# Optimization experiments

Measured on AMD Instinct MI355X. Metric: run time of the kernel, lower is better.

## Reference

```python
import jax, jax.numpy as jnp
import numpy as np

B, C, H, W = 4, 128, 256, 256
N, NPOS, KS = 4000, 8, 3
CH = 2 * NPOS  # mask=False -> 2*n_pos offset channels


def setup_inputs() -> dict:
    key = jax.random.key(0)
    ks = jax.random.split(key, 8)
    x = jax.random.normal(ks[0], (B, C, H, W), jnp.float32)
    keypoints = jax.random.uniform(ks[1], (B, N, 2), jnp.float32) * 2.0 - 1.0  # [-1,1]
    w1 = jax.random.normal(ks[2], (CH, C, KS, KS), jnp.float32) * 0.05  # offset conv 3x3
    b1 = jnp.zeros((CH,), jnp.float32)
    w2 = jax.random.normal(ks[3], (CH, CH), jnp.float32) * 0.05        # offset conv 1x1
    b2 = jnp.zeros((CH,), jnp.float32)
    wsf = jax.random.normal(ks[4], (C, C), jnp.float32) * 0.05         # sf_conv 1x1 no bias
    agg_weights = jax.random.uniform(ks[5], (NPOS, C, C), jnp.float32)  # torch.rand init
    return {"x": x, "keypoints": keypoints, "w1": w1, "b1": b1, "w2": w2,
            "b2": b2, "wsf": wsf, "agg_weights": agg_weights}


def _bilinear_sample(img, px, py):
    """grid_sample(mode=bilinear, align_corners=True, padding=zeros) at pixel coords.
    img: (C,H,W); px,py: (M,). Returns (C,M)."""
    c, h, w = img.shape
    x0f = jnp.floor(px); y0f = jnp.floor(py)
    x0 = x0f.astype(jnp.int32); y0 = y0f.astype(jnp.int32)
    wx1 = px - x0f; wx0 = 1.0 - wx1
    wy1 = py - y0f; wy0 = 1.0 - wy1

    def tap(xi, yi, wgt):
        valid = ((xi >= 0) & (xi < w) & (yi >= 0) & (yi < h)).astype(img.dtype)
        v = img[:, jnp.clip(yi, 0, h - 1), jnp.clip(xi, 0, w - 1)]  # (C,M)
        return v * (wgt * valid)

    return (tap(x0, y0, wx0 * wy0) + tap(x0 + 1, y0, wx1 * wy0)
            + tap(x0, y0 + 1, wx0 * wy1) + tap(x0 + 1, y0 + 1, wx1 * wy1))


def _per_image(xi, kpts, w1, b1, w2, b2, wsf, agg_weights):
    wh = jnp.array([W - 1.0, H - 1.0], xi.dtype)
    max_offset = max(H, W) / 4.0
    kwh = (kpts / 2.0 + 0.5) * wh                      # (N,2) pixel coords, >=0
    rc = kwh.astype(jnp.int32)                          # .long() trunc (positive)
    corner = jnp.trunc(rc.astype(jnp.float32) - KS / 2.0 + 1.0).astype(jnp.int32)
    cx = jnp.clip(corner[:, 0], 0, W - 1 - KS)
    cy = jnp.clip(corner[:, 1], 0, H - 1 - KS)
    ar = jnp.arange(KS)
    # patch[n,c,a,b] = xi[c, cy_n+a, cx_n+b]
    patch = xi[:, (cy[:, None] + ar)[:, :, None], (cx[:, None] + ar)[:, None, :]]  # (C,N,KS,KS)
    patch = patch.transpose(1, 0, 2, 3)                 # (N,C,KS,KS)
    # offset network: 3x3 conv (valid) on 3x3 patch == full contraction, then ReLU, 1x1 conv
    h1 = jax.nn.relu(jnp.einsum('nchw,ochw->no', patch, w1) + b1)
    off = jnp.clip(h1 @ w2.T + b2, -max_offset, max_offset)  # (N, 2*NPOS)
    off = off.reshape(-1, 2, NPOS).transpose(0, 2, 1)        # (N,NPOS,2)
    # deform sampling positions; torch normalizes then grid_sample(align_corners=True)
    # maps exactly back to pixel coords, so sample at pixel coords directly
    pos = kwh[:, None, :] + off                              # (N,NPOS,2)
    feats = _bilinear_sample(xi, pos[..., 0].reshape(-1), pos[..., 1].reshape(-1))  # (C,N*NPOS)
    feats = feats.reshape(C, -1, NPOS).transpose(1, 0, 2)    # (N,C,NPOS)
    feats = jax.nn.selu(jnp.einsum('ncp,dc->ndp', feats, wsf))
    descs = jnp.einsum('ncp,pcd->nd', feats, agg_weights)    # (N,C)
    descs = descs / jnp.maximum(jnp.linalg.norm(descs, axis=1, keepdims=True), 1e-12)
    return descs, off


def reference(x, keypoints, w1, b1, w2, b2, wsf, agg_weights):
    f = jax.vmap(lambda xi, k: _per_image(xi, k, w1, b1, w2, b2, wsf, agg_weights))
    descriptors, offsets = f(x, keypoints)
    return descriptors, offsets  # (B,N,C), (B,N,NPOS,2)
```

## Files before the change

kernel.cpp:

```cpp
#include <hip/hip_runtime.h>
#include <math.h>

#define BB 4
#define CC 128
#define HH 256
#define WW 256
#define NN 4000
#define NPOS 8
#define KS 3
#define HWSZ (HH*WW)

#define SELU_ALPHA 1.6732632423543772f
#define SELU_SCALE 1.0507009873554805f
#define MAX_OFFSET 64.0f

typedef unsigned short ushort_t;
typedef short short8 __attribute__((ext_vector_type(8)));
typedef float f32x4 __attribute__((ext_vector_type(4)));
typedef unsigned short ushort4_t __attribute__((ext_vector_type(4)));

#define XT_ELEMS    ((size_t)BB*HH*WW*CC)
#define WSFBF_ELEMS ((size_t)CC*CC)
#define AGGT_ELEMS  ((size_t)NPOS*CC*CC)
#define W1T_ELEMS   ((size_t)16*CC*9)
#define WS_NEEDED   ((XT_ELEMS+WSFBF_ELEMS+AGGT_ELEMS+W1T_ELEMS)*sizeof(ushort_t))

__device__ __forceinline__ ushort_t f2bf(float f) {
    unsigned u = __builtin_bit_cast(unsigned, f);
    unsigned r = (u + 0x7FFFu + ((u >> 16) & 1u)) >> 16;
    return (ushort_t)r;
}
__device__ __forceinline__ float bf2f(ushort_t u) {
    return __builtin_bit_cast(float, ((unsigned)u) << 16);
}

__global__ __launch_bounds__(256) void k0p(
    const float* __restrict__ x, ushort_t* __restrict__ xt,
    const float* __restrict__ wsf, const float* __restrict__ agg,
    const float* __restrict__ w1,
    ushort_t* __restrict__ wsf_bf, ushort_t* __restrict__ aggT_bf,
    ushort_t* __restrict__ w1t_bf)
{
    int blk = blockIdx.x;
    const int t = threadIdx.x;
    if (blk >= BB * HH * 4) {
        int i = (blk - BB * HH * 4) * 256 + t;
        if (i < CC * CC) wsf_bf[i] = f2bf(wsf[i]);
        if (i < NPOS * CC * CC) {
            int p = i >> 14, d = (i >> 7) & 127, c = i & 127;
            aggT_bf[i] = f2bf(agg[(p << 14) + (c << 7) + d]);
        }
        if (i < 16 * 1152) {
            int o = i / 1152, e = i - o * 1152, k = e >> 7, c = e & 127;
            w1t_bf[i] = f2bf(w1[o * 1152 + c * 9 + k]);
        }
        return;
    }
    int xc = blk & 3, y = (blk >> 2) & 255, b = blk >> 10;
    int x0 = xc * 64;
    __shared__ ushort_t lds[64][136];

    const float* xb = x + (size_t)b * CC * HWSZ + (size_t)y * WW + x0;
    for (int v = t; v < 2048; v += 256) {
        int c = v >> 4, xo4 = v & 15;
        float4 val = *(const float4*)(xb + (size_t)c * HWSZ + xo4 * 4);
        lds[xo4*4+0][c] = f2bf(val.x);
        lds[xo4*4+1][c] = f2bf(val.y);
        lds[xo4*4+2][c] = f2bf(val.z);
        lds[xo4*4+3][c] = f2bf(val.w);
    }
    __syncthreads();
    ushort_t* outb = xt + ((size_t)b * HWSZ + (size_t)y * WW + x0) * CC;
    for (int v = t; v < 2048; v += 256) {
        int xo = v >> 5, c4 = v & 31;
        ushort4_t val;
        val[0] = lds[xo][c4*4+0];
        val[1] = lds[xo][c4*4+1];
        val[2] = lds[xo][c4*4+2];
        val[3] = lds[xo][c4*4+3];
        *(ushort4_t*)(outb + (size_t)xo * CC + c4 * 4) = val;
    }
}

__global__ __launch_bounds__(256, 2) void k14_fused(
    const ushort_t* __restrict__ xt, const float* __restrict__ kpts,
    const ushort_t* __restrict__ w1t_bf, const float* __restrict__ b1,
    const float* __restrict__ w2, const float* __restrict__ b2,
    const ushort_t* __restrict__ wsf_bf, const ushort_t* __restrict__ aggT_bf,
    float* __restrict__ out_desc, float* __restrict__ out_off)
{
    const int t    = threadIdx.x;
    const int wv   = t >> 6;
    const int lane = t & 63;
    const int m    = lane & 15;
    const int q    = lane >> 4;
    const int n0   = blockIdx.x * 16;
    const int b    = n0 / NN;
    const ushort_t* xb = xt + (size_t)b * HWSZ * CC;

    __shared__ ushort_t feats[CC * CC];
    __shared__ ushort_t g[CC * CC];
    __shared__ union {
        struct {
            float partials[4][16][16];
            float h1f[16][17];
            float offs[16][16];
            int   tapoff[128][4];
            float tapw[128][4];
        } a;
        float dbuf[16 * 132];
    } u;
    __shared__ float kw[16][2];
    __shared__ int   cxy[16][2];
    __shared__ float rn[16];

    if (t < 16) {
        float kx = kpts[(size_t)(n0 + t) * 2 + 0];
        float ky = kpts[(size_t)(n0 + t) * 2 + 1];
        float kwx = (kx * 0.5f + 0.5f) * (float)(WW - 1);
        float kwy = (ky * 0.5f + 0.5f) * (float)(HH - 1);
        kw[t][0] = kwx; kw[t][1] = kwy;
        int rcx = (int)kwx, rcy = (int)kwy;
        int cx = (int)truncf((float)rcx - 0.5f);
        int cy = (int)truncf((float)rcy - 0.5f);
        cxy[t][0] = min(max(cx, 0), WW - 1 - KS);
        cxy[t][1] = min(max(cy, 0), HH - 1 - KS);
    }
    __syncthreads();

    {
        int px0 = cxy[m][0], py0 = cxy[m][1];
        f32x4 hacc = {0.f, 0.f, 0.f, 0.f};
        const ushort_t* brow = w1t_bf + m * 1152 + wv * 288 + q * 8;
        #pragma unroll
        for (int kk = 0; kk < 9; ++kk) {
            int e = wv * 288 + kk * 32 + q * 8;
            int k = e >> 7, c = e & 127;
            int kd = k / 3, kx2 = k - kd * 3;
            const ushort_t* src = xb + ((size_t)((py0 + kd) * WW + px0 + kx2)) * CC + c;
            short8 a   = *(const short8*)src;
            short8 bfr = *(const short8*)(brow + kk * 32);
            hacc = __builtin_amdgcn_mfma_f32_16x16x32_bf16(a, bfr, hacc, 0, 0, 0);
        }
        #pragma unroll
        for (int r = 0; r < 4; ++r) u.a.partials[wv][q * 4 + r][m] = hacc[r];
    }
    __syncthreads();
    {
        int kp = t >> 4, o = t & 15;
        float h = u.a.partials[0][kp][o] + u.a.partials[1][kp][o]
                + u.a.partials[2][kp][o] + u.a.partials[3][kp][o] + b1[o];
        u.a.h1f[kp][o] = fmaxf(h, 0.f);
    }
    __syncthreads();
    {
        int kp = t >> 4, j = t & 15;
        float s = b2[j];
        #pragma unroll
        for (int o = 0; o < 16; ++o) s += u.a.h1f[kp][o] * w2[j * 16 + o];
        s = fminf(fmaxf(s, -MAX_OFFSET), MAX_OFFSET);
        u.a.offs[kp][j] = s;
        int p = j & 7, comp = j >> 3;
        out_off[((size_t)(n0 + kp) * 8 + p) * 2 + comp] = s;
    }
    __syncthreads();

    if (t < 128) {
        int kp = t >> 3, p = t & 7;
        float px = kw[kp][0] + u.a.offs[kp][p];
        float py = kw[kp][1] + u.a.offs[kp][8 + p];
        float x0f = floorf(px), y0f = floorf(py);
        int x0 = (int)x0f, y0 = (int)y0f;
        float wx1 = px - x0f, wx0 = 1.f - wx1;
        float wy1 = py - y0f, wy0 = 1.f - wy1;
        int x0c = min(max(x0, 0), WW - 1);
        int x1c = min(max(x0 + 1, 0), WW - 1);
        int y0c = min(max(y0, 0), HH - 1);
        int y1c = min(max(y0 + 1, 0), HH - 1);
        float vx0 = (x0 >= 0 && x0 < WW) ? 1.f : 0.f;
        float vx1 = (x0 + 1 >= 0 && x0 + 1 < WW) ? 1.f : 0.f;
        float vy0 = (y0 >= 0 && y0 < HH) ? 1.f : 0.f;
        float vy1 = (y0 + 1 >= 0 && y0 + 1 < HH) ? 1.f : 0.f;
        u.a.tapoff[t][0] = (y0c * WW + x0c) * CC;
        u.a.tapoff[t][1] = (y0c * WW + x1c) * CC;
        u.a.tapoff[t][2] = (y1c * WW + x0c) * CC;
        u.a.tapoff[t][3] = (y1c * WW + x1c) * CC;
        u.a.tapw[t][0] = wx0 * wy0 * vx0 * vy0;
        u.a.tapw[t][1] = wx1 * wy0 * vx1 * vy0;
        u.a.tapw[t][2] = wx0 * wy1 * vx0 * vy1;
        u.a.tapw[t][3] = wx1 * wy1 * vx1 * vy1;
    }
    __syncthreads();

    {
        int pair = t >> 1, half = t & 1;
        const ushort_t* s0 = xb + u.a.tapoff[pair][0];
        const ushort_t* s1 = xb + u.a.tapoff[pair][1];
        const ushort_t* s2 = xb + u.a.tapoff[pair][2];
        const ushort_t* s3 = xb + u.a.tapoff[pair][3];
        float w00 = u.a.tapw[pair][0], w01 = u.a.tapw[pair][1];
        float w10 = u.a.tapw[pair][2], w11 = u.a.tapw[pair][3];
        unsigned rbase = (unsigned)(pair * 256);
        unsigned key   = ((unsigned)(pair & 7)) << 4;
        #pragma unroll
        for (int i = 0; i < 16; ++i) {
            int c = half * 64 + i * 4;
            ushort4_t t0 = *(const ushort4_t*)(s0 + c);
            ushort4_t t1 = *(const ushort4_t*)(s1 + c);
            ushort4_t t2 = *(const ushort4_t*)(s2 + c);
            ushort4_t t3 = *(const ushort4_t*)(s3 + c);
            ushort4_t r4;
            #pragma unroll
            for (int j = 0; j < 4; ++j) {
                float v = bf2f(t0[j]) * w00 + bf2f(t1[j]) * w01
                        + bf2f(t2[j]) * w10 + bf2f(t3[j]) * w11;
                r4[j] = f2bf(v);
            }
            unsigned byte = (rbase + (unsigned)c * 2) ^ key;
            *(ushort4_t*)((char*)feats + byte) = r4;
        }
    }
    __syncthreads();

    for (int rti = 0; rti < 2; ++rti) {
        int rt = wv * 2 + rti;
        int r  = rt * 16 + m;
        unsigned key = ((unsigned)(r & 7)) << 4;
        short8 afr[4];
        #pragma unroll
        for (int kk = 0; kk < 4; ++kk) {
            unsigned byte = ((unsigned)(r * 256 + q * 16 + kk * 64)) ^ key;
            afr[kk] = *(const short8*)((const char*)feats + byte);
        }
        for (int ct = 0; ct < 8; ++ct) {
            const ushort_t* brow = wsf_bf + (ct * 16 + m) * CC + q * 8;
            f32x4 acc = {0.f, 0.f, 0.f, 0.f};
            #pragma unroll
            for (int kk = 0; kk < 4; ++kk) {
                short8 bfr = *(const short8*)(brow + kk * 32);
                acc = __builtin_amdgcn_mfma_f32_16x16x32_bf16(afr[kk], bfr, acc, 0, 0, 0);
            }
            #pragma unroll
            for (int rr = 0; rr < 4; ++rr) {
                float s = acc[rr];
                s = (s > 0.f) ? (SELU_SCALE * s)
                              : (SELU_SCALE * SELU_ALPHA * (expf(s) - 1.f));
                int row = rt * 16 + q * 4 + rr;
                int col = ct * 16 + m;
                unsigned byte = ((unsigned)(row * 256 + col * 2))
                              ^ (((unsigned)((row >> 3) & 7)) << 4);
                *(ushort_t*)((char*)g + byte) = f2bf(s);
            }
        }
    }
    __syncthreads();

    f32x4 acc2[2];
    acc2[0] = (f32x4){0.f, 0.f, 0.f, 0.f};
    acc2[1] = (f32x4){0.f, 0.f, 0.f, 0.f};
    const int ctbase = wv * 2;
    for (int kk = 0; kk < 32; ++kk) {
        int p    = kk >> 2;
        int rowA = m * 8 + p;
        unsigned byte = ((unsigned)(rowA * 256 + (kk & 3) * 64 + q * 16))
                      ^ (((unsigned)((rowA >> 3) & 7)) << 4);
        short8 afr = *(const short8*)((const char*)g + byte);
        #pragma unroll
        for (int i = 0; i < 2; ++i) {
            int ct = ctbase + i;
            const ushort_t* brow = aggT_bf + (size_t)(p * CC + ct * 16 + m) * CC
                                 + (kk & 3) * 32 + q * 8;
            short8 bfr = *(const short8*)brow;
            acc2[i] = __builtin_amdgcn_mfma_f32_16x16x32_bf16(afr, bfr, acc2[i], 0, 0, 0);
        }
    }
    #pragma unroll
    for (int i = 0; i < 2; ++i) {
        int ct = ctbase + i;
        #pragma unroll
        for (int rr = 0; rr < 4; ++rr) {
            int n = q * 4 + rr;
            u.dbuf[n * 132 + ct * 16 + m] = acc2[i][rr];
        }
    }
    __syncthreads();

    {
        int n = t >> 4, l = t & 15;
        float s = 0.f;
        #pragma unroll
        for (int j = 0; j < 8; ++j) { float v = u.dbuf[n * 132 + l + j * 16]; s += v * v; }
        s += __shfl_xor(s, 1);
        s += __shfl_xor(s, 2);
        s += __shfl_xor(s, 4);
        s += __shfl_xor(s, 8);
        if (l == 0) rn[n] = 1.0f / fmaxf(sqrtf(s), 1e-12f);
    }
    __syncthreads();
    for (int idx = t; idx < 2048; idx += 256) {
        int n = idx >> 7, d = idx & 127;
        out_desc[(size_t)(n0 + n) * CC + d] = u.dbuf[n * 132 + d] * rn[n];
    }
}

__global__ __launch_bounds__(256, 4) void sddh_baseline(
    const float* __restrict__ x, const float* __restrict__ keypoints,
    const float* __restrict__ w1, const float* __restrict__ b1,
    const float* __restrict__ w2, const float* __restrict__ b2,
    const float* __restrict__ wsf, const float* __restrict__ agg,
    float* __restrict__ out_desc, float* __restrict__ out_off)
{
    const int bn = blockIdx.x;
    const int b  = bn / NN;
    const int t  = threadIdx.x;
    const float* xi = x + (size_t)b * CC * HWSZ;

    __shared__ float patch[CC * 9];
    __shared__ float conv_part[16][17];
    __shared__ float h1s[16];
    __shared__ float offs[16];
    __shared__ float feats[CC][NPOS];
    __shared__ float cpart2[CC][NPOS];
    __shared__ float g[CC][NPOS];
    __shared__ float dpart[CC];
    __shared__ float desc[CC];
    __shared__ float sq[128];
    __shared__ float kxy[2];

    if (t == 0) {
        float kx = keypoints[(size_t)bn * 2 + 0];
        float ky = keypoints[(size_t)bn * 2 + 1];
        kxy[0] = (kx * 0.5f + 0.5f) * (float)(WW - 1);
        kxy[1] = (ky * 0.5f + 0.5f) * (float)(HH - 1);
    }
    __syncthreads();
    const float kwx = kxy[0], kwy = kxy[1];
    const int rcx = (int)kwx, rcy = (int)kwy;
    int cx = (int)truncf((float)rcx - 0.5f);
    int cy = (int)truncf((float)rcy - 0.5f);
    cx = min(max(cx, 0), WW - 1 - KS);
    cy = min(max(cy, 0), HH - 1 - KS);

    for (int e = t; e < CC * 9; e += 256) {
        int c = e / 9, k = e % 9;
        int dy = k / 3, dx = k % 3;
        patch[e] = xi[(size_t)c * HWSZ + (cy + dy) * WW + (cx + dx)];
    }
    __syncthreads();
    {
        int o = t & 15, j = t >> 4;
        float acc = 0.f;
        const float* wo = w1 + o * (CC * 9);
        for (int e = j; e < CC * 9; e += 16) acc += patch[e] * wo[e];
        conv_part[o][j] = acc;
    }
    __syncthreads();
    if (t < 16) {
        float s = b1[t];
        #pragma unroll
        for (int j = 0; j < 16; j++) s += conv_part[t][j];
        h1s[t] = fmaxf(s, 0.f);
    }
    __syncthreads();
    if (t < 16) {
        float s = b2[t];
        #pragma unroll
        for (int k = 0; k < 16; k++) s += h1s[k] * w2[t * 16 + k];
        s = fminf(fmaxf(s, -MAX_OFFSET), MAX_OFFSET);
        offs[t] = s;
        int idx = (t < 8) ? (bn * 16 + t * 2) : (bn * 16 + (t - 8) * 2 + 1);
        out_off[idx] = s;
    }
    __syncthreads();

    for (int e = t; e < CC * NPOS; e += 256) {
        int c = e & 127, p = e >> 7;
        float px = kwx + offs[p];
        float py = kwy + offs[8 + p];
        float x0f = floorf(px), y0f = floorf(py);
        int x0 = (int)x0f, y0 = (int)y0f;
        float wx1 = px - x0f, wx0 = 1.f - wx1;
        float wy1 = py - y0f, wy0 = 1.f - wy1;
        const float* xc = xi + (size_t)c * HWSZ;
        int x0c = min(max(x0, 0), WW - 1);
        int x1c = min(max(x0 + 1, 0), WW - 1);
        int y0c = min(max(y0, 0), HH - 1);
        int y1c = min(max(y0 + 1, 0), HH - 1);
        float vx0 = (x0 >= 0 && x0 < WW) ? 1.f : 0.f;
        float vx1 = (x0 + 1 >= 0 && x0 + 1 < WW) ? 1.f : 0.f;
        float vy0 = (y0 >= 0 && y0 < HH) ? 1.f : 0.f;
        float vy1 = (y0 + 1 >= 0 && y0 + 1 < HH) ? 1.f : 0.f;
        float v = 0.f;
        v += xc[y0c * WW + x0c] * (wx0 * wy0) * (vx0 * vy0);
        v += xc[y0c * WW + x1c] * (wx1 * wy0) * (vx1 * vy0);
        v += xc[y1c * WW + x0c] * (wx0 * wy1) * (vx0 * vy1);
        v += xc[y1c * WW + x1c] * (wx1 * wy1) * (vx1 * vy1);
        feats[c][p] = v;
    }
    __syncthreads();
    {
        int d = t & 127, chalf = t >> 7;
        float acc[NPOS];
        #pragma unroll
        for (int p = 0; p < NPOS; p++) acc[p] = 0.f;
        const float* wrow = wsf + d * CC;
        int c0 = chalf * 64;
        for (int c = c0; c < c0 + 64; c++) {
            float wv = wrow[c];
            #pragma unroll
            for (int p = 0; p < NPOS; p++) acc[p] += feats[c][p] * wv;
        }
        if (chalf) {
            #pragma unroll
            for (int p = 0; p < NPOS; p++) cpart2[d][p] = acc[p];
        }
        __syncthreads();
        if (!chalf) {
            #pragma unroll
            for (int p = 0; p < NPOS; p++) {
                float s = acc[p] + cpart2[d][p];
                s = (s > 0.f) ? (SELU_SCALE * s)
                              : (SELU_SCALE * SELU_ALPHA * (expf(s) - 1.f));
                g[d][p] = s;
            }
        }
    }
    __syncthreads();
    {
        int d = t & 127, half = t >> 7;
        float acc = 0.f;
        int p0 = half * 4;
        for (int p = p0; p < p0 + 4; p++) {
            const float* ap = agg + (size_t)p * CC * CC;
            for (int e = 0; e < CC; e++) acc += g[e][p] * ap[e * CC + d];
        }
        if (half) dpart[d] = acc;
        __syncthreads();
        if (!half) {
            float v = acc + dpart[d];
            desc[d] = v;
            sq[d] = v * v;
        }
    }
    __syncthreads();
    if (t < 64) sq[t] += sq[t + 64]; __syncthreads();
    if (t < 32) sq[t] += sq[t + 32]; __syncthreads();
    if (t < 16) sq[t] += sq[t + 16]; __syncthreads();
    if (t < 8)  sq[t] += sq[t + 8];  __syncthreads();
    if (t < 4)  sq[t] += sq[t + 4];  __syncthreads();
    if (t < 2)  sq[t] += sq[t + 2];  __syncthreads();
    if (t == 0) sq[0] = fmaxf(sqrtf(sq[0] + sq[1]), 1e-12f);
    __syncthreads();
    if (t < 128) out_desc[(size_t)bn * CC + t] = desc[t] / sq[0];
}

extern "C" void kernel_launch(void* const* d_in, const int* in_sizes, int n_in,
                              void* d_out, int out_size, void* d_ws, size_t ws_size,
                              hipStream_t stream) {
    const float* x    = (const float*)d_in[0];
    const float* kpts = (const float*)d_in[1];
    const float* w1   = (const float*)d_in[2];
    const float* b1   = (const float*)d_in[3];
    const float* w2   = (const float*)d_in[4];
    const float* b2   = (const float*)d_in[5];
    const float* wsf  = (const float*)d_in[6];
    const float* agg  = (const float*)d_in[7];

    float* out_desc = (float*)d_out;
    float* out_off  = (float*)d_out + (size_t)BB * NN * CC;

    if (ws_size < WS_NEEDED) {
        hipLaunchKernelGGL(sddh_baseline, dim3(BB * NN), dim3(256), 0, stream,
                           x, kpts, w1, b1, w2, b2, wsf, agg, out_desc, out_off);
        return;
    }

    ushort_t* xt      = (ushort_t*)d_ws;
    ushort_t* wsf_bf  = xt + XT_ELEMS;
    ushort_t* aggT_bf = wsf_bf + WSFBF_ELEMS;
    ushort_t* w1t_bf  = aggT_bf + AGGT_ELEMS;

    hipLaunchKernelGGL(k0p, dim3(BB * HH * 4 + 512), dim3(256), 0, stream,
                       x, xt, wsf, agg, w1, wsf_bf, aggT_bf, w1t_bf);
    hipLaunchKernelGGL(k14_fused, dim3(BB * NN / 16), dim3(256), 0, stream,
                       xt, kpts, w1t_bf, b1, w2, b2, wsf_bf, aggT_bf,
                       out_desc, out_off);
}
```

Before: 106.8 us.

## Merge feats and g LDS buffers, compute norms from registers, raise occupancy

Aliases the bilinear-sampled feature buffer and the SELU output buffer into one 32KB LDS array, which drops per-block shared memory from about 64KB+ to about 36KB. Launch bounds go from 2 to 4 blocks per SIMD. The L2 normalisation now reduces sums of squares straight from MFMA accumulators with shuffles instead of staging through an LDS buffer. The gather channel interleave is also changed. The risks are a read/write race on the shared buffer: the SELU stage writes g rows while other waves may still be reading feats rows, since only the per-wave afr registers are loaded first. There is also register pressure from the tighter launch bound.

New measurement: 118.1 us. 10.6% more time.

```diff
diff --git a/kernel.cpp b/kernel.cpp
--- a/kernel.cpp
+++ b/kernel.cpp
@@ -82,7 +82,7 @@
     }
 }
 
-__global__ __launch_bounds__(256, 2) void k14_fused(
+__global__ __launch_bounds__(256, 4) void k14_fused(
     const ushort_t* __restrict__ xt, const float* __restrict__ kpts,
     const ushort_t* __restrict__ w1t_bf, const float* __restrict__ b1,
     const float* __restrict__ w2, const float* __restrict__ b2,
@@ -98,20 +98,17 @@
     const int b    = n0 / NN;
     const ushort_t* xb = xt + (size_t)b * HWSZ * CC;
 
-    __shared__ ushort_t feats[CC * CC];
-    __shared__ ushort_t g[CC * CC];
-    __shared__ union {
-        struct {
-            float partials[4][16][16];
-            float h1f[16][17];
-            float offs[16][16];
-            int   tapoff[128][4];
-            float tapw[128][4];
-        } a;
-        float dbuf[16 * 132];
-    } u;
+    __shared__ ushort_t fg[CC * CC];
+    union PT {
+        float partials[4][16][16];
+        struct { int tapoff[128][4]; float tapw[128][4]; } tp;
+    };
+    __shared__ PT    upt;
+    __shared__ float h1f[16][17];
+    __shared__ float offs[16][16];
     __shared__ float kw[16][2];
     __shared__ int   cxy[16][2];
+    __shared__ float wsum[4][16];
     __shared__ float rn[16];
 
     if (t < 16) {
@@ -143,23 +140,23 @@
             hacc = __builtin_amdgcn_mfma_f32_16x16x32_bf16(a, bfr, hacc, 0, 0, 0);
         }
         #pragma unroll
-        for (int r = 0; r < 4; ++r) u.a.partials[wv][q * 4 + r][m] = hacc[r];
+        for (int r = 0; r < 4; ++r) upt.partials[wv][q * 4 + r][m] = hacc[r];
     }
     __syncthreads();
     {
         int kp = t >> 4, o = t & 15;
-        float h = u.a.partials[0][kp][o] + u.a.partials[1][kp][o]
-                + u.a.partials[2][kp][o] + u.a.partials[3][kp][o] + b1[o];
-        u.a.h1f[kp][o] = fmaxf(h, 0.f);
+        float h = upt.partials[0][kp][o] + upt.partials[1][kp][o]
+                + upt.partials[2][kp][o] + upt.partials[3][kp][o] + b1[o];
+        h1f[kp][o] = fmaxf(h, 0.f);
     }
     __syncthreads();
     {
         int kp = t >> 4, j = t & 15;
         float s = b2[j];
         #pragma unroll
-        for (int o = 0; o < 16; ++o) s += u.a.h1f[kp][o] * w2[j * 16 + o];
+        for (int o = 0; o < 16; ++o) s += h1f[kp][o] * w2[j * 16 + o];
         s = fminf(fmaxf(s, -MAX_OFFSET), MAX_OFFSET);
-        u.a.offs[kp][j] = s;
+        offs[kp][j] = s;
         int p = j & 7, comp = j >> 3;
         out_off[((size_t)(n0 + kp) * 8 + p) * 2 + comp] = s;
     }
@@ -167,8 +164,8 @@
 
     if (t < 128) {
         int kp = t >> 3, p = t & 7;
-        float px = kw[kp][0] + u.a.offs[kp][p];
-        float py = kw[kp][1] + u.a.offs[kp][8 + p];
+        float px = kw[kp][0] + offs[kp][p];
+        float py = kw[kp][1] + offs[kp][8 + p];
         float x0f = floorf(px), y0f = floorf(py);
         int x0 = (int)x0f, y0 = (int)y0f;
         float wx1 = px - x0f, wx0 = 1.f - wx1;
@@ -181,30 +178,30 @@
         float vx1 = (x0 + 1 >= 0 && x0 + 1 < WW) ? 1.f : 0.f;
         float vy0 = (y0 >= 0 && y0 < HH) ? 1.f : 0.f;
         float vy1 = (y0 + 1 >= 0 && y0 + 1 < HH) ? 1.f : 0.f;
-        u.a.tapoff[t][0] = (y0c * WW + x0c) * CC;
-        u.a.tapoff[t][1] = (y0c * WW + x1c) * CC;
-        u.a.tapoff[t][2] = (y1c * WW + x0c) * CC;
-        u.a.tapoff[t][3] = (y1c * WW + x1c) * CC;
-        u.a.tapw[t][0] = wx0 * wy0 * vx0 * vy0;
-        u.a.tapw[t][1] = wx1 * wy0 * vx1 * vy0;
-        u.a.tapw[t][2] = wx0 * wy1 * vx0 * vy1;
-        u.a.tapw[t][3] = wx1 * wy1 * vx1 * vy1;
+        upt.tp.tapoff[t][0] = (y0c * WW + x0c) * CC;
+        upt.tp.tapoff[t][1] = (y0c * WW + x1c) * CC;
+        upt.tp.tapoff[t][2] = (y1c * WW + x0c) * CC;
+        upt.tp.tapoff[t][3] = (y1c * WW + x1c) * CC;
+        upt.tp.tapw[t][0] = wx0 * wy0 * vx0 * vy0;
+        upt.tp.tapw[t][1] = wx1 * wy0 * vx1 * vy0;
+        upt.tp.tapw[t][2] = wx0 * wy1 * vx0 * vy1;
+        upt.tp.tapw[t][3] = wx1 * wy1 * vx1 * vy1;
     }
     __syncthreads();
 
     {
         int pair = t >> 1, half = t & 1;
-        const ushort_t* s0 = xb + u.a.tapoff[pair][0];
-        const ushort_t* s1 = xb + u.a.tapoff[pair][1];
-        const ushort_t* s2 = xb + u.a.tapoff[pair][2];
-        const ushort_t* s3 = xb + u.a.tapoff[pair][3];
-        float w00 = u.a.tapw[pair][0], w01 = u.a.tapw[pair][1];
-        float w10 = u.a.tapw[pair][2], w11 = u.a.tapw[pair][3];
+        const ushort_t* s0 = xb + upt.tp.tapoff[pair][0];
+        const ushort_t* s1 = xb + upt.tp.tapoff[pair][1];
+        const ushort_t* s2 = xb + upt.tp.tapoff[pair][2];
+        const ushort_t* s3 = xb + upt.tp.tapoff[pair][3];
+        float w00 = upt.tp.tapw[pair][0], w01 = upt.tp.tapw[pair][1];
+        float w10 = upt.tp.tapw[pair][2], w11 = upt.tp.tapw[pair][3];
         unsigned rbase = (unsigned)(pair * 256);
         unsigned key   = ((unsigned)(pair & 7)) << 4;
         #pragma unroll
         for (int i = 0; i < 16; ++i) {
-            int c = half * 64 + i * 4;
+            int c = i * 8 + half * 4;
             ushort4_t t0 = *(const ushort4_t*)(s0 + c);
             ushort4_t t1 = *(const ushort4_t*)(s1 + c);
             ushort4_t t2 = *(const ushort4_t*)(s2 + c);
@@ -217,7 +214,7 @@
                 r4[j] = f2bf(v);
             }
             unsigned byte = (rbase + (unsigned)c * 2) ^ key;
-            *(ushort4_t*)((char*)feats + byte) = r4;
+            *(ushort4_t*)((char*)fg + byte) = r4;
         }
     }
     __syncthreads();
@@ -230,7 +227,7 @@
         #pragma unroll
         for (int kk = 0; kk < 4; ++kk) {
             unsigned byte = ((unsigned)(r * 256 + q * 16 + kk * 64)) ^ key;
-            afr[kk] = *(const short8*)((const char*)feats + byte);
+            afr[kk] = *(const short8*)((const char*)fg + byte);
         }
         for (int ct = 0; ct < 8; ++ct) {
             const ushort_t* brow = wsf_bf + (ct * 16 + m) * CC + q * 8;
@@ -249,7 +246,7 @@
                 int col = ct * 16 + m;
                 unsigned byte = ((unsigned)(row * 256 + col * 2))
                               ^ (((unsigned)((row >> 3) & 7)) << 4);
-                *(ushort_t*)((char*)g + byte) = f2bf(s);
+                *(ushort_t*)((char*)fg + byte) = f2bf(s);
             }
         }
     }
@@ -264,7 +261,7 @@
         int rowA = m * 8 + p;
         unsigned byte = ((unsigned)(rowA * 256 + (kk & 3) * 64 + q * 16))
                       ^ (((unsigned)((rowA >> 3) & 7)) << 4);
-        short8 afr = *(const short8*)((const char*)g + byte);
+        short8 afr = *(const short8*)((const char*)fg + byte);
         #pragma unroll
         for (int i = 0; i < 2; ++i) {
             int ct = ctbase + i;
@@ -274,32 +271,38 @@
             acc2[i] = __builtin_amdgcn_mfma_f32_16x16x32_bf16(afr, bfr, acc2[i], 0, 0, 0);
         }
     }
-    #pragma unroll
-    for (int i = 0; i < 2; ++i) {
-        int ct = ctbase + i;
-        #pragma unroll
-        for (int rr = 0; rr < 4; ++rr) {
-            int n = q * 4 + rr;
-            u.dbuf[n * 132 + ct * 16 + m] = acc2[i][rr];
-        }
-    }
-    __syncthreads();
-
-    {
-        int n = t >> 4, l = t & 15;
-        float s = 0.f;
-        #pragma unroll
-        for (int j = 0; j < 8; ++j) { float v = u.dbuf[n * 132 + l + j * 16]; s += v * v; }
-        s += __shfl_xor(s, 1);
-        s += __shfl_xor(s, 2);
-        s += __shfl_xor(s, 4);
-        s += __shfl_xor(s, 8);
-        if (l == 0) rn[n] = 1.0f / fmaxf(sqrtf(s), 1e-12f);
-    }
-    __syncthreads();
-    for (int idx = t; idx < 2048; idx += 256) {
-        int n = idx >> 7, d = idx & 127;
-        out_desc[(size_t)(n0 + n) * CC + d] = u.dbuf[n * 132 + d] * rn[n];
+
+    {
+        float ss[4];
+        #pragma unroll
+        for (int rr = 0; rr < 4; ++rr)
+            ss[rr] = acc2[0][rr] * acc2[0][rr] + acc2[1][rr] * acc2[1][rr];
+        #pragma unroll
+        for (int mask = 1; mask <= 8; mask <<= 1) {
+            #pragma unroll
+            for (int rr = 0; rr < 4; ++rr) ss[rr] += __shfl_xor(ss[rr], mask);
+        }
+        if (m == 0) {
+            #pragma unroll
+            for (int rr = 0; rr < 4; ++rr) wsum[wv][q * 4 + rr] = ss[rr];
+        }
+    }
+    __syncthreads();
+    if (t < 16) {
+        float tot = wsum[0][t] + wsum[1][t] + wsum[2][t] + wsum[3][t];
+        rn[t] = 1.0f / fmaxf(sqrtf(tot), 1e-12f);
+    }
+    __syncthreads();
+    {
+        #pragma unroll
+        for (int i = 0; i < 2; ++i) {
+            int col = (ctbase + i) * 16 + m;
+            #pragma unroll
+            for (int rr = 0; rr < 4; ++rr) {
+                int n = q * 4 + rr;
+                out_desc[(size_t)(n0 + n) * CC + col] = acc2[i][rr] * rn[n];
+            }
+        }
     }
 }
 
```
